# Kernel optimization log

Hardware: AMD Instinct MI355X
Metric: run time of the kernel (lower is better)

The kernel has to match this reference:

```python
import math
import jax, jax.numpy as jnp
import numpy as np

B, T, C, H = 4, 2048, 1024, 1024

def setup_inputs() -> dict:
    key = jax.random.key(0)
    kx, kk, kq, kv = jax.random.split(key, 4)
    s = 1.0 / math.sqrt(C)
    return {
        "x": jax.random.normal(kx, (B, T, C), dtype=jnp.float32),
        # torch Linear weight is [out, in]; store transposed [in, out] for x @ W
        "Wk": jax.random.uniform(kk, (C, H), dtype=jnp.float32, minval=-s, maxval=s),
        "Wq": jax.random.uniform(kq, (C, H), dtype=jnp.float32, minval=-s, maxval=s),
        "Wv": jax.random.uniform(kv, (C, H), dtype=jnp.float32, minval=-s, maxval=s),
    }

def reference(x, Wk, Wq, Wv):
    K = x @ Wk  # [B,T,H]
    Q = x @ Wq
    V = x @ Wv
    scale = 1.0 / math.sqrt(K.shape[-1])
    wei = jnp.einsum('bth,bsh->bts', Q, K) * scale  # [B,T,T]
    t = x.shape[1]
    causal = jnp.tril(jnp.ones((t, t), dtype=bool))
    wei = jnp.where(causal, wei, -jnp.inf)
    wei = jax.nn.softmax(wei, axis=-1)
    wei = jax.nn.relu(wei)  # no-op mathematically but kept for fidelity
    return jnp.einsum('bts,bsh->bth', wei, V)
```

## Files before the change

### kernel.cpp

```cpp
#include <hip/hip_runtime.h>

typedef _Float16 f16;
typedef _Float16 f16x8 __attribute__((ext_vector_type(8)));
typedef float    f32x4 __attribute__((ext_vector_type(4)));

#define AS3 __attribute__((address_space(3)))
#define AS1 __attribute__((address_space(1)))

static __device__ __forceinline__ void gld_lds16(const f16* g, f16* l) {
    __builtin_amdgcn_global_load_lds((const AS1 void*)g, (AS3 void*)l, 16, 0, 0);
}


__global__ void cvt_x(const float* __restrict__ x, f16* __restrict__ xh) {
    int i = blockIdx.x * blockDim.x + threadIdx.x;
    const f32x4* xv = (const f32x4*)x;
    f32x4 a = xv[2 * i], b = xv[2 * i + 1];
    f16x8 h;
    h[0] = (f16)a[0]; h[1] = (f16)a[1]; h[2] = (f16)a[2]; h[3] = (f16)a[3];
    h[4] = (f16)b[0]; h[5] = (f16)b[1]; h[6] = (f16)b[2]; h[7] = (f16)b[3];
    ((f16x8*)xh)[i] = h;
}

__global__ void cvt_transpose_w(const float* __restrict__ Wq, const float* __restrict__ Wk,
                                const float* __restrict__ Wv, f16* __restrict__ Wt) {
    const float* W = blockIdx.z == 0 ? Wq : (blockIdx.z == 1 ? Wk : Wv);
    __shared__ float tile[32][33];
    int tx = threadIdx.x, ty = threadIdx.y;
    int n0 = blockIdx.x * 32, k0 = blockIdx.y * 32;
#pragma unroll
    for (int r = 0; r < 4; ++r)
        tile[ty + r * 8][tx] = W[(size_t)(k0 + ty + r * 8) * 1024 + n0 + tx];
    __syncthreads();
    f16* o = Wt + (size_t)blockIdx.z * 1024 * 1024;
#pragma unroll
    for (int r = 0; r < 4; ++r)
        o[(size_t)(n0 + ty + r * 8) * 1024 + k0 + tx] = (f16)tile[tx][ty + r * 8];
}

template <int MODE>
__global__ __launch_bounds__(256, 4)
void gemm128(const f16* __restrict__ A, int lda, long aStride,
             const f16* __restrict__ B, int ldb, long bStride,
             void* __restrict__ Cout, int ldc, long cStride,
             int ktiles, float scale, float* __restrict__ lsum,
             const f16* __restrict__ A2, const f16* __restrict__ B2,
             void* __restrict__ C2) {
    int bm, bn, bz = blockIdx.z;
    int m0, n0;
    const f16 *Ab, *Bb;
    char* Cb;

    if (MODE == 0) {
        bn = blockIdx.x; bm = blockIdx.y;
        n0 = bn * 128;
        if (bm < 64) {
            m0 = bm * 128;
            Ab = A; Bb = B; Cb = (char*)Cout;
        } else {
            int t = bm - 64;
            int bb = t >> 3;
            m0 = (t & 7) * 128;
            Ab = A2;
            Bb = B2 + (long)bb * 2048 * 1024;
            Cb = (char*)C2 + (long)bb * 1024 * 2048 * sizeof(f16);
        }
    } else if (MODE == 1) {
        int i = blockIdx.x;
        float ff = sqrtf(8.f * (float)i + 1.f);
        bm = (int)((ff - 1.f) * 0.5f);
        while ((bm + 1) * (bm + 2) / 2 <= i) ++bm;
        while (bm * (bm + 1) / 2 > i) --bm;
        bn = i - bm * (bm + 1) / 2;
        m0 = bm * 128; n0 = bn * 128;
        Ab = A + (long)bz * aStride;
        Bb = B + (long)bz * bStride;
        Cb = (char*)Cout + (long)bz * cStride * sizeof(f16);
    } else {
        bn = blockIdx.x; bm = gridDim.y - 1 - blockIdx.y;
        int lim = 4 * (bm + 1); if (lim < ktiles) ktiles = lim;
        m0 = bm * 128; n0 = bn * 128;
        Ab = A + (long)bz * aStride;
        Bb = B + (long)bz * bStride;
        Cb = (char*)Cout + (long)bz * cStride * sizeof(float);
    }

    __shared__ f16 lds[2 * 8192];

    const int tid = threadIdx.x;
    const int wave = tid >> 6, lane = tid & 63;
    const int q = lane >> 4, rr = lane & 15;
    const int wm = (wave >> 1) * 64, wn = (wave & 1) * 64;

    const f16* pA = Ab + (long)(m0 + (tid >> 2)) * lda + (tid & 3) * 8;
    const f16* pB = Bb + (long)(n0 + (tid >> 2)) * ldb + (tid & 3) * 8;

    auto stage = [&](int kt, int buf) {
        const int k0 = kt * 32;
        f16* lA = lds + buf * 8192 + wave * 512;
        f16* lB = lds + buf * 8192 + 4096 + wave * 512;
#pragma unroll
        for (int it = 0; it < 2; ++it) {
            gld_lds16(pA + (long)it * 64 * lda + k0, lA + it * 2048);
            gld_lds16(pB + (long)it * 64 * ldb + k0, lB + it * 2048);
        }
    };

    f32x4 acc[4][4] = {};

    stage(0, 0);
    __syncthreads();

    for (int kt = 0; kt < ktiles; ++kt) {
        const int cur = kt & 1;
        if (kt + 1 < ktiles) stage(kt + 1, 1 - cur);
        const f16* bufA = lds + cur * 8192;
        const f16* bufB = bufA + 4096;
        f16x8 af[4], bf[4];
#pragma unroll
        for (int i = 0; i < 4; ++i)
            af[i] = *(const f16x8*)&bufA[(wm + i * 16 + rr) * 32 + q * 8];
#pragma unroll
        for (int j = 0; j < 4; ++j)
            bf[j] = *(const f16x8*)&bufB[(wn + j * 16 + rr) * 32 + q * 8];
#pragma unroll
        for (int i = 0; i < 4; ++i)
#pragma unroll
            for (int j = 0; j < 4; ++j)
                acc[i][j] = __builtin_amdgcn_mfma_f32_16x16x32_f16(af[i], bf[j], acc[i][j], 0, 0, 0);
        __syncthreads();
    }

#pragma unroll
    for (int i = 0; i < 4; ++i) {
#pragma unroll
        for (int r2 = 0; r2 < 4; ++r2) {
            const int row = wm + i * 16 + q * 4 + r2;
            float psum = 0.f;
            float inv = 1.f;
            if (MODE == 2) inv = 1.0f / lsum[bz * 2048 + m0 + row];
#pragma unroll
            for (int j = 0; j < 4; ++j) {
                const int col = wn + j * 16 + rr;
                float v = acc[i][j][r2] * scale;
                long idx = (long)(m0 + row) * ldc + n0 + col;
                if (MODE == 1) {
                    v = __expf(v);
                    if (n0 + col > m0 + row) v = 0.f;
                    psum += v;
                    ((f16*)Cb)[idx] = (f16)v;
                } else if (MODE == 0) {
                    ((f16*)Cb)[idx] = (f16)v;
                } else {
                    ((float*)Cb)[idx] = v * inv;
                }
            }
            if (MODE == 1) {
                psum += __shfl_xor(psum, 1, 64);
                psum += __shfl_xor(psum, 2, 64);
                psum += __shfl_xor(psum, 4, 64);
                psum += __shfl_xor(psum, 8, 64);
                if (rr == 0) atomicAdd(&lsum[bz * 2048 + m0 + row], psum);
            }
        }
    }
}

extern "C" void kernel_launch(void* const* d_in, const int* in_sizes, int n_in,
                              void* d_out, int out_size, void* d_ws, size_t ws_size,
                              hipStream_t stream) {
    (void)in_sizes; (void)n_in; (void)out_size; (void)ws_size;
    const float* x  = (const float*)d_in[0];
    const float* Wk = (const float*)d_in[1];
    const float* Wq = (const float*)d_in[2];
    const float* Wv = (const float*)d_in[3];
    float* out = (float*)d_out;

    const long MB = 1l << 20;
    char* ws = (char*)d_ws;
    f16*   qk   = (f16*)(ws);
    f16*   Vt   = (f16*)(ws + 32 * MB);
    f16*   P    = (f16*)(ws + 48 * MB);
    float* lsum = (float*)(ws + 80 * MB);
    f16*   xh   = (f16*)(ws + 81 * MB);
    f16*   Wt   = (f16*)(ws + 97 * MB);

    cvt_x<<<4096, 256, 0, stream>>>(x, xh);
    cvt_transpose_w<<<dim3(32, 32, 3), dim3(32, 8), 0, stream>>>(Wq, Wk, Wv, Wt);
    hipMemsetAsync(lsum, 0, 4 * 2048 * sizeof(float), stream);

    gemm128<0><<<dim3(16, 96, 1), 256, 0, stream>>>(xh, 1024, 0, Wt, 1024, 0,
                                                    qk, 2048, 0, 32, 1.0f, nullptr,
                                                    Wt + 2l * 1024 * 1024, xh, Vt);
    gemm128<1><<<dim3(136, 1, 4), 256, 0, stream>>>(qk, 2048, 2048l * 2048,
                                                    qk + 1024, 2048, 2048l * 2048,
                                                    P, 2048, 2048l * 2048, 32, 0.03125f, lsum,
                                                    nullptr, nullptr, nullptr);
    gemm128<2><<<dim3(8, 16, 4), 256, 0, stream>>>(P, 2048, 2048l * 2048,
                                                   Vt, 2048, 1024l * 2048,
                                                   out, 1024, 2048l * 1024, 64, 1.0f, lsum,
                                                   nullptr, nullptr, nullptr);
}
```

Baseline: 244.8 us.

## Replace LDS-staged GEMM tiles with direct register loads and double-buffered fragments

Removes the shared-memory staging (global_load_lds plus barriers) and has each wave load its MFMA operand fragments straight from global memory into registers, double-buffering two k-tiles in registers. Launch bounds drop to 3 blocks per CU to make room for the extra registers. This removes LDS traffic and syncthreads, but tiles are no longer shared between waves, so each A/B fragment is fetched twice from global/L2 and access patterns become 16-byte strided rows. It also assumes ktiles is even.

```diff
diff --git a/kernel.cpp b/kernel.cpp
--- a/kernel.cpp
+++ b/kernel.cpp
@@ -3,13 +3,6 @@
 typedef _Float16 f16;
 typedef _Float16 f16x8 __attribute__((ext_vector_type(8)));
 typedef float    f32x4 __attribute__((ext_vector_type(4)));
-
-#define AS3 __attribute__((address_space(3)))
-#define AS1 __attribute__((address_space(1)))
-
-static __device__ __forceinline__ void gld_lds16(const f16* g, f16* l) {
-    __builtin_amdgcn_global_load_lds((const AS1 void*)g, (AS3 void*)l, 16, 0, 0);
-}
 
 
 __global__ void cvt_x(const float* __restrict__ x, f16* __restrict__ xh) {
@@ -39,7 +32,7 @@
 }
 
 template <int MODE>
-__global__ __launch_bounds__(256, 4)
+__global__ __launch_bounds__(256, 3)
 void gemm128(const f16* __restrict__ A, int lda, long aStride,
              const f16* __restrict__ B, int ldb, long bStride,
              void* __restrict__ Cout, int ldc, long cStride,
@@ -85,51 +78,47 @@
         Cb = (char*)Cout + (long)bz * cStride * sizeof(float);
     }
 
-    __shared__ f16 lds[2 * 8192];
-
     const int tid = threadIdx.x;
     const int wave = tid >> 6, lane = tid & 63;
     const int q = lane >> 4, rr = lane & 15;
     const int wm = (wave >> 1) * 64, wn = (wave & 1) * 64;
 
-    const f16* pA = Ab + (long)(m0 + (tid >> 2)) * lda + (tid & 3) * 8;
-    const f16* pB = Bb + (long)(n0 + (tid >> 2)) * ldb + (tid & 3) * 8;
+    const f16* pA = Ab + (long)(m0 + wm + rr) * lda + q * 8;
+    const f16* pB = Bb + (long)(n0 + wn + rr) * ldb + q * 8;
 
-    auto stage = [&](int kt, int buf) {
-        const int k0 = kt * 32;
-        f16* lA = lds + buf * 8192 + wave * 512;
-        f16* lB = lds + buf * 8192 + 4096 + wave * 512;
-#pragma unroll
-        for (int it = 0; it < 2; ++it) {
-            gld_lds16(pA + (long)it * 64 * lda + k0, lA + it * 2048);
-            gld_lds16(pB + (long)it * 64 * ldb + k0, lB + it * 2048);
-        }
-    };
-
+    f16x8 af[2][4], bf[2][4];
     f32x4 acc[4][4] = {};
 
-    stage(0, 0);
-    __syncthreads();
+#define LOADF(kt, buf)                                                        \
+    {                                                                         \
+        const int k0_ = (kt) * 32;                                            \
+        _Pragma("unroll")                                                     \
+        for (int i_ = 0; i_ < 4; ++i_) {                                      \
+            af[buf][i_] = *(const f16x8*)(pA + (long)i_ * 16 * lda + k0_);    \
+            bf[buf][i_] = *(const f16x8*)(pB + (long)i_ * 16 * ldb + k0_);    \
+        }                                                                     \
+    }
 
-    for (int kt = 0; kt < ktiles; ++kt) {
-        const int cur = kt & 1;
-        if (kt + 1 < ktiles) stage(kt + 1, 1 - cur);
-        const f16* bufA = lds + cur * 8192;
-        const f16* bufB = bufA + 4096;
-        f16x8 af[4], bf[4];
-#pragma unroll
-        for (int i = 0; i < 4; ++i)
-            af[i] = *(const f16x8*)&bufA[(wm + i * 16 + rr) * 32 + q * 8];
-#pragma unroll
-        for (int j = 0; j < 4; ++j)
-            bf[j] = *(const f16x8*)&bufB[(wn + j * 16 + rr) * 32 + q * 8];
-#pragma unroll
-        for (int i = 0; i < 4; ++i)
-#pragma unroll
-            for (int j = 0; j < 4; ++j)
-                acc[i][j] = __builtin_amdgcn_mfma_f32_16x16x32_f16(af[i], bf[j], acc[i][j], 0, 0, 0);
-        __syncthreads();
+#define MFMA_STEP(buf)                                                        \
+    {                                                                         \
+        _Pragma("unroll")                                                     \
+        for (int i_ = 0; i_ < 4; ++i_)                                        \
+            _Pragma("unroll")                                                 \
+            for (int j_ = 0; j_ < 4; ++j_)                                    \
+                acc[i_][j_] = __builtin_amdgcn_mfma_f32_16x16x32_f16(         \
+                    af[buf][i_], bf[buf][j_], acc[i_][j_], 0, 0, 0);          \
     }
+
+    LOADF(0, 0);
+    LOADF(1, 1);
+    for (int kt = 0; kt < ktiles; kt += 2) {
+        MFMA_STEP(0);
+        if (kt + 2 < ktiles) LOADF(kt + 2, 0);
+        MFMA_STEP(1);
+        if (kt + 3 < ktiles) LOADF(kt + 3, 1);
+    }
+#undef LOADF
+#undef MFMA_STEP
 
 #pragma unroll
     for (int i = 0; i < 4; ++i) {
```

Result: slower. 474.9 us (+94.0%).
